# Kernel tuning notes

Hardware: AMD Instinct MI355X
Metric: run time of the kernel (lower is better)

The kernel has to match this reference:

```python
import jax, jax.numpy as jnp
import numpy as np

B, N, K, H = 4, 2048, 30, 8
NUM_HIDDEN, NUM_IN, NUM_LATENT = 512, 640, 128
D = NUM_HIDDEN // H


def setup_inputs() -> dict:
    key = jax.random.key(0)
    ks = jax.random.split(key, 10)
    s = 0.05
    return {
        "z": jax.random.normal(ks[0], (B, NUM_LATENT), jnp.float32),
        "h_V": jax.random.normal(ks[1], (B, N, NUM_HIDDEN), jnp.float32),
        "h_E": jax.random.normal(ks[2], (B, N, K, NUM_IN), jnp.float32),
        "mask_attend": jnp.ones((B, N, K), jnp.float32),
        # weights stored as (in, out); torch Linear computes x @ W.T
        "W_Q": jax.random.normal(ks[3], (NUM_HIDDEN, NUM_HIDDEN), jnp.float32) * s,
        "W_K": jax.random.normal(ks[4], (NUM_IN, NUM_HIDDEN), jnp.float32) * s,
        "W_V": jax.random.normal(ks[5], (NUM_IN, NUM_HIDDEN), jnp.float32) * s,
        "W_O": jax.random.normal(ks[6], (NUM_HIDDEN, NUM_HIDDEN), jnp.float32) * s,
        "W_z": jax.random.normal(ks[7], (NUM_LATENT, K * H), jnp.float32) * s,
        "W_b": jax.random.normal(ks[8], (NUM_IN - 33, H), jnp.float32) * s,
    }


def reference(z, h_V, h_E, mask_attend, W_Q, W_K, W_V, W_O, W_z, W_b):
    b, n, k, _ = h_E.shape
    # projections
    Q = (h_V @ W_Q).reshape(b, n, H, D)            # [B,N,H,D]
    Kp = (h_E @ W_K).reshape(b, n, k, H, D)        # [B,N,K,H,D]
    V = (h_E @ W_V).reshape(b, n, k, H, D)         # [B,N,K,H,D]
    # per-neighbor dot-product scores -> [B,N,H,K]
    logits = jnp.einsum("bnhd,bnkhd->bnhk", Q, Kp) / np.sqrt(D).astype(np.float32)
    # latent bias: W_z output reshaped as (K, H) then transposed -> [B,1,H,K]
    bias_latent = (z @ W_z).reshape(b, 1, k, H).transpose(0, 1, 3, 2)
    # edge bias from h_E features past index 33 -> [B,N,H,K]
    bias_edges = (h_E[..., 33:] @ W_b).reshape(b, n, k, H).transpose(0, 1, 3, 2)
    logits = logits + bias_latent + bias_edges
    # masked, numerically stable softmax over K neighbors
    mask = mask_attend[:, :, None, :]              # [B,N,1,K] broadcast over heads
    neg_inf = jnp.finfo(jnp.float32).min
    logits = jnp.where(mask > 0, logits, neg_inf)
    attend = jax.nn.softmax(logits, axis=-1) * mask  # [B,N,H,K]
    # weighted aggregation of V, merge heads, output projection
    h_upd = jnp.einsum("bnhk,bnkhd->bnhd", attend, V).reshape(b, n, NUM_HIDDEN)
    return h_upd @ W_O
```

## Files before the change

### kernel.cpp

```cpp
#include <hip/hip_runtime.h>

#define B_      4
#define N_      2048
#define KN      30
#define H_      8
#define D_      64
#define CH      512
#define CI      640
#define CL      128
#define BN_TOT  8192

typedef unsigned short u16;
typedef unsigned int   u32;

typedef __attribute__((ext_vector_type(8))) short bf16x8;
typedef __attribute__((ext_vector_type(4))) float f32x4;

__device__ __forceinline__ float bf2f(u16 u) {
    return __uint_as_float(((u32)u) << 16);
}
__device__ __forceinline__ u16 f2bf(float f) {
    u32 u = __float_as_uint(f);
    return (u16)((u + 0x7FFFu + ((u >> 16) & 1u)) >> 16);
}

#define NEG_INF (-3.4028234663852886e38f)

__device__ __forceinline__ void async16(const void* g, void* l) {
    __builtin_amdgcn_global_load_lds(
        (const __attribute__((address_space(1))) unsigned int*)g,
        (__attribute__((address_space(3))) unsigned int*)l, 16, 0, 0);
}

__global__ __launch_bounds__(256) void cvt_kernel(
    const float* __restrict__ in, u16* __restrict__ out, int n)
{
    int i4 = (blockIdx.x * 256 + threadIdx.x) * 4;
    if (i4 < n) {
        float4 v = *(const float4*)&in[i4];
        ushort4 s;
        s.x = f2bf(v.x); s.y = f2bf(v.y); s.z = f2bf(v.z); s.w = f2bf(v.w);
        *(ushort4*)&out[i4] = s;
    }
}

__global__ __launch_bounds__(256) void cvt_t_kernel(
    const float* __restrict__ in, u16* __restrict__ out, int R, int Cc)
{
    int o = blockIdx.x * 256 + threadIdx.x;
    if (o < R * Cc) {
        int j = o / R, i = o - j * R;
        out[o] = f2bf(in[(size_t)i * Cc + j]);
    }
}

template<int BN, bool BF16OUT, bool WBIAS>
__global__ __launch_bounds__(256) void mfma_gemm(
    const u16* __restrict__ A, const u16* __restrict__ Bt, void* __restrict__ Cp,
    int K, int lda, int ldb, int ldc,
    long aHead, long bHead, long cHead, float alpha,
    const float* __restrict__ wb)
{
    constexpr int WN = BN / 2;
    constexpr int NT = WN / 16;
    constexpr int BR = (BN * 4) / 256;

    __shared__ u16 lA[128 * 32];
    __shared__ u16 lB[BN * 32];

    const int t    = threadIdx.x;
    const int w    = t >> 6;
    const int lane = t & 63;
    const int fr   = lane & 15;
    const int fq   = lane >> 4;
    const int wm   = w >> 1, wn = w & 1;
    const int m0   = blockIdx.y * 128;
    const int n0   = blockIdx.x * BN;

    const u16* Ah = A  + (size_t)blockIdx.z * aHead;
    const u16* Bh = Bt + (size_t)blockIdx.z * bHead;

    f32x4 zero = {0.f, 0.f, 0.f, 0.f};
    f32x4 acc[4][NT];
#pragma unroll
    for (int i = 0; i < 4; i++)
#pragma unroll
        for (int j = 0; j < NT; j++) acc[i][j] = zero;

    for (int k0 = 0; k0 < K; k0 += 32) {
#pragma unroll
        for (int r = 0; r < 2; r++) {
            int chunk = r * 256 + t;
            async16(Ah + (size_t)(m0 + (chunk >> 2)) * lda + k0 + ((chunk & 3) << 3),
                    &lA[(r * 256 + w * 64) * 8]);
        }
#pragma unroll
        for (int r = 0; r < BR; r++) {
            int chunk = r * 256 + t;
            async16(Bh + (size_t)(n0 + (chunk >> 2)) * ldb + k0 + ((chunk & 3) << 3),
                    &lB[(r * 256 + w * 64) * 8]);
        }
        __syncthreads();

        bf16x8 af[4], bfr[NT];
#pragma unroll
        for (int i = 0; i < 4; i++)
            af[i] = *(const bf16x8*)&lA[(wm * 64 + i * 16 + fr) * 32 + fq * 8];
#pragma unroll
        for (int j = 0; j < NT; j++)
            bfr[j] = *(const bf16x8*)&lB[(wn * WN + j * 16 + fr) * 32 + fq * 8];
#pragma unroll
        for (int i = 0; i < 4; i++)
#pragma unroll
            for (int j = 0; j < NT; j++)
                acc[i][j] = __builtin_amdgcn_mfma_f32_16x16x32_bf16(
                    af[i], bfr[j], acc[i][j], 0, 0, 0);
        __syncthreads();
    }

    const size_t cbase = (size_t)blockIdx.z * cHead;
#pragma unroll
    for (int i = 0; i < 4; i++) {
        int row = m0 + wm * 64 + i * 16 + fq * 4;
#pragma unroll
        for (int j = 0; j < NT; j++) {
            int col = n0 + wn * WN + j * 16 + fr;
#pragma unroll
            for (int r = 0; r < 4; r++) {
                float v = acc[i][j][r] * alpha;
                if (WBIAS) {
                    if (col >= 33) v += wb[(size_t)(col - 33) * H_ + blockIdx.z];
                }
                if (BF16OUT)
                    ((u16*)Cp)[cbase + (size_t)(row + r) * ldc + col] = f2bf(v);
                else
                    ((float*)Cp)[cbase + (size_t)(row + r) * ldc + col] = v;
            }
        }
    }
}

__global__ __launch_bounds__(256) void biasl_kernel(
    const float* __restrict__ z, const float* __restrict__ Wz,
    float* __restrict__ biasL)
{
    const int t = threadIdx.x;
    if (t < KN * H_) {
        for (int b = 0; b < B_; b++) {
            float s = 0.f;
            for (int l = 0; l < CL; l++) s += z[b * CL + l] * Wz[l * (KN * H_) + t];
            biasL[b * (KN * H_) + t] = s;
        }
    }
}

__global__ __launch_bounds__(256) void attn_kernel(
    const float* __restrict__ hE, const float* __restrict__ mask,
    const u16* Qt, const float* __restrict__ biasL, u16* Eagg)
{
    __shared__ __align__(16) u16 ehs[KN * CI];
    __shared__ __align__(16) u16 lqt[H_ * CI];
    __shared__ float logit_s[H_ * 32];
    __shared__ float att_s[KN * H_];
    __shared__ float mask_s[KN];

    const int bn   = blockIdx.x;
    const int b    = bn >> 11;
    const int t    = threadIdx.x;
    const int w    = t >> 6;
    const int lane = t & 63;
    const int fr   = lane & 15;
    const int fq   = lane >> 4;
    char* ebase = (char*)ehs;
    char* qbase = (char*)lqt;

    const float* he = hE + (size_t)bn * KN * CI;
    {
        int idx = t;
#pragma unroll 6
        for (int it = 0; it < 18; ++it, idx += 256) {
            int k = idx / 160;
            int c = (idx - k * 160) << 2;
            float4 v = *(const float4*)&he[k * CI + c];
            ushort4 sv;
            sv.x = f2bf(v.x); sv.y = f2bf(v.y); sv.z = f2bf(v.z); sv.w = f2bf(v.w);
            *(ushort4*)(ebase + ((k * 1280 + (c << 1)) ^ ((k & 7) << 4))) = sv;
        }
        if (t < 192) {
            int idx2 = 4608 + t;
            int k = idx2 / 160;
            int c = (idx2 - k * 160) << 2;
            float4 v = *(const float4*)&he[k * CI + c];
            ushort4 sv;
            sv.x = f2bf(v.x); sv.y = f2bf(v.y); sv.z = f2bf(v.z); sv.w = f2bf(v.w);
            *(ushort4*)(ebase + ((k * 1280 + (c << 1)) ^ ((k & 7) << 4))) = sv;
        }
    }
    {
        const u16* qg = Qt + (size_t)bn * (H_ * CI);
        for (int idx = t; idx < 640; idx += 256) {
            int row = idx / 80;
            bf16x8 v = *(const bf16x8*)(qg + idx * 8);
            *(bf16x8*)(qbase + ((idx * 16) ^ ((row & 7) << 4))) = v;
        }
    }
    if (t < KN) mask_s[t] = mask[(size_t)bn * KN + t];
    __syncthreads();

    if (w < 2) {
        const int h8   = fr & 7;
        const int qswz = h8 << 4;
        int nr = w * 16 + fr;
        if (nr > KN - 1) nr = KN - 1;
        const char* erow = ebase + nr * 1280;
        const int swz = (nr & 7) << 4;
        f32x4 lacc = {0.f, 0.f, 0.f, 0.f};
#pragma unroll 4
        for (int kk = 0; kk < CI / 32; kk++) {
            bf16x8 a  = *(const bf16x8*)(qbase + ((h8 * 1280 + kk * 64 + fq * 16) ^ qswz));
            bf16x8 bf = *(const bf16x8*)(erow + ((kk * 64 + fq * 16) ^ swz));
            lacc = __builtin_amdgcn_mfma_f32_16x16x32_bf16(a, bf, lacc, 0, 0, 0);
        }
        int k = w * 16 + fr;
        if (fq < 2 && k < KN) {
            float mk = mask_s[k];
            const float* blp = &biasL[b * (KN * H_) + k * H_];
#pragma unroll
            for (int r = 0; r < 4; r++) {
                int h = fq * 4 + r;
                float lg = lacc[r] + blp[h];
                logit_s[h * 32 + k] = (mk > 0.f) ? lg : NEG_INF;
            }
        }
    }
    __syncthreads();

    if (t < 64) {
        const int h  = t >> 3;
        const int kg = t & 7;
        float lv[4];
#pragma unroll
        for (int i = 0; i < 4; i++) {
            int k = kg * 4 + i;
            float v = logit_s[h * 32 + k];
            lv[i] = (k < KN) ? v : NEG_INF;
        }
        float m = fmaxf(fmaxf(lv[0], lv[1]), fmaxf(lv[2], lv[3]));
        m = fmaxf(m, __shfl_xor(m, 1));
        m = fmaxf(m, __shfl_xor(m, 2));
        m = fmaxf(m, __shfl_xor(m, 4));
        float e[4], s = 0.f;
#pragma unroll
        for (int i = 0; i < 4; i++) { e[i] = __expf(lv[i] - m); s += e[i]; }
        s += __shfl_xor(s, 1);
        s += __shfl_xor(s, 2);
        s += __shfl_xor(s, 4);
        float inv = 1.f / s;
#pragma unroll
        for (int i = 0; i < 4; i++) {
            int k = kg * 4 + i;
            if (k < KN) att_s[k * H_ + h] = e[i] * inv * mask_s[k];
        }
    }
    __syncthreads();

    if (t < 160) {
        const int c0 = t << 2;
        float acc[8][4] = {};
        for (int k = 0; k < KN; k++) {
            ushort4 ev = *(const ushort4*)(ebase + ((k * 1280 + (c0 << 1)) ^ ((k & 7) << 4)));
            float f0 = bf2f(ev.x), f1 = bf2f(ev.y), f2 = bf2f(ev.z), f3 = bf2f(ev.w);
            float4 a0 = *(const float4*)&att_s[k * H_];
            float4 a1 = *(const float4*)&att_s[k * H_ + 4];
            float aw[8] = {a0.x, a0.y, a0.z, a0.w, a1.x, a1.y, a1.z, a1.w};
#pragma unroll
            for (int h = 0; h < 8; h++) {
                acc[h][0] += aw[h] * f0; acc[h][1] += aw[h] * f1;
                acc[h][2] += aw[h] * f2; acc[h][3] += aw[h] * f3;
            }
        }
#pragma unroll
        for (int h = 0; h < 8; h++) {
            ushort4 sv;
            sv.x = f2bf(acc[h][0]); sv.y = f2bf(acc[h][1]);
            sv.z = f2bf(acc[h][2]); sv.w = f2bf(acc[h][3]);
            *(ushort4*)&Eagg[((size_t)bn * H_ + h) * CI + c0] = sv;
        }
    }
}

extern "C" void kernel_launch(void* const* d_in, const int* in_sizes, int n_in,
                              void* d_out, int out_size, void* d_ws, size_t ws_size,
                              hipStream_t stream)
{
    const float* z    = (const float*)d_in[0];
    const float* hV   = (const float*)d_in[1];
    const float* hE   = (const float*)d_in[2];
    const float* mask = (const float*)d_in[3];
    const float* WQ   = (const float*)d_in[4];
    const float* WK   = (const float*)d_in[5];
    const float* WV   = (const float*)d_in[6];
    const float* WO   = (const float*)d_in[7];
    const float* Wz   = (const float*)d_in[8];
    const float* Wb   = (const float*)d_in[9];
    float* out = (float*)d_out;

    char* w = (char*)d_ws;
    u16*   hV_bf = (u16*)w;
    u16*   Q_bf  = (u16*)(w + 8388608);
    u16*   Qt    = (u16*)(w + 16777216);
    u16*   WQt   = (u16*)(w + 100663296);
    u16*   WK_bf = (u16*)(w + 101187584);
    u16*   WVt   = (u16*)(w + 101842944);
    u16*   WOt   = (u16*)(w + 102498304);
    float* biasL = (float*)(w + 103022592);
    u16*   Eagg  = Qt;
    u16*   Hupd  = hV_bf;

    cvt_kernel<<<4096, 256, 0, stream>>>(hV, hV_bf, BN_TOT * CH);
    cvt_kernel<<<320, 256, 0, stream>>>(WK, WK_bf, CI * CH);
    cvt_t_kernel<<<1024, 256, 0, stream>>>(WQ, WQt, CH, CH);
    cvt_t_kernel<<<1280, 256, 0, stream>>>(WV, WVt, CI, CH);
    cvt_t_kernel<<<1024, 256, 0, stream>>>(WO, WOt, CH, CH);
    biasl_kernel<<<1, 256, 0, stream>>>(z, Wz, biasL);

    mfma_gemm<128, true, false><<<dim3(4, 64, 1), 256, 0, stream>>>(
        hV_bf, WQt, Q_bf, CH, CH, CH, CH, 0, 0, 0, 1.0f, nullptr);
    mfma_gemm<128, true, true><<<dim3(5, 64, H_), 256, 0, stream>>>(
        Q_bf, WK_bf, Qt, 64, CH, CH, H_ * CI, 64, 64, CI, 0.125f, Wb);
    attn_kernel<<<dim3(BN_TOT), 256, 0, stream>>>(hE, mask, Qt, biasL, Eagg);
    mfma_gemm<64, true, false><<<dim3(1, 64, H_), 256, 0, stream>>>(
        Eagg, WVt, Hupd, CI, H_ * CI, CI, CH, CI, 64L * CI, 64, 1.0f, nullptr);
    mfma_gemm<128, false, false><<<dim3(4, 64, 1), 256, 0, stream>>>(
        Hupd, WOt, out, CH, CH, CH, CH, 0, 0, 0, 1.0f, nullptr);
}
```

Baseline: 1.061 ms.

## Use MFMA for attention-weighted edge aggregation and packed bf16 conversion in attn kernel

The per-node attention kernel now computes the weighted sum of edge features over 30 neighbours with bf16 MFMA (16x16x32) instead of scalar FP32 FMAs on 160 threads, storing attention weights as bf16 padded to 32 neighbours and 16 rows. Edge loading is reorganised so each thread handles a neighbour row, uses the packed v_cvt_pk_bf16_f32 conversion and a two-level XOR swizzle, and zero-fills padding rows. Q is read directly from global memory instead of being staged in LDS, which frees shared memory. Attention weights now pass through bf16, which loses some precision. The B operand is gathered with eight scalar 16-bit LDS reads per MFMA, and the output is written as scattered 16-bit stores.

```diff
diff --git a/kernel.cpp b/kernel.cpp
--- a/kernel.cpp
+++ b/kernel.cpp
@@ -23,6 +23,14 @@
     u32 u = __float_as_uint(f);
     return (u16)((u + 0x7FFFu + ((u >> 16) & 1u)) >> 16);
 }
+__device__ __forceinline__ u32 pk2bf(float lo, float hi) {
+    u32 r;
+    asm("v_cvt_pk_bf16_f32 %0, %1, %2" : "=v"(r) : "v"(lo), "v"(hi));
+    return r;
+}
+__device__ __forceinline__ u16 f2bf1(float f) {
+    return (u16)pk2bf(f, f);
+}
 
 #define NEG_INF (-3.4028234663852886e38f)
 
@@ -158,10 +166,9 @@
     const float* __restrict__ hE, const float* __restrict__ mask,
     const u16* Qt, const float* __restrict__ biasL, u16* Eagg)
 {
-    __shared__ __align__(16) u16 ehs[KN * CI];
-    __shared__ __align__(16) u16 lqt[H_ * CI];
+    __shared__ __align__(16) u16 ehs[32 * CI];
     __shared__ float logit_s[H_ * 32];
-    __shared__ float att_s[KN * H_];
+    __shared__ __align__(8) u16 att_b[16 * 32];
     __shared__ float mask_s[KN];
 
     const int bn   = blockIdx.x;
@@ -172,52 +179,44 @@
     const int fr   = lane & 15;
     const int fq   = lane >> 4;
     char* ebase = (char*)ehs;
-    char* qbase = (char*)lqt;
 
     const float* he = hE + (size_t)bn * KN * CI;
     {
-        int idx = t;
-#pragma unroll 6
-        for (int it = 0; it < 18; ++it, idx += 256) {
-            int k = idx / 160;
-            int c = (idx - k * 160) << 2;
-            float4 v = *(const float4*)&he[k * CI + c];
-            ushort4 sv;
-            sv.x = f2bf(v.x); sv.y = f2bf(v.y); sv.z = f2bf(v.z); sv.w = f2bf(v.w);
-            *(ushort4*)(ebase + ((k * 1280 + (c << 1)) ^ ((k & 7) << 4))) = sv;
-        }
-        if (t < 192) {
-            int idx2 = 4608 + t;
-            int k = idx2 / 160;
-            int c = (idx2 - k * 160) << 2;
-            float4 v = *(const float4*)&he[k * CI + c];
-            ushort4 sv;
-            sv.x = f2bf(v.x); sv.y = f2bf(v.y); sv.z = f2bf(v.z); sv.w = f2bf(v.w);
-            *(ushort4*)(ebase + ((k * 1280 + (c << 1)) ^ ((k & 7) << 4))) = sv;
-        }
-    }
-    {
-        const u16* qg = Qt + (size_t)bn * (H_ * CI);
-        for (int idx = t; idx < 640; idx += 256) {
-            int row = idx / 80;
-            bf16x8 v = *(const bf16x8*)(qg + idx * 8);
-            *(bf16x8*)(qbase + ((idx * 16) ^ ((row & 7) << 4))) = v;
+        const int kr = t >> 3;
+        const int c8 = t & 7;
+        char* wrow = ebase + kr * 1280;
+        const u32 swz = (u32)(((kr & 7) << 4) ^ ((kr & 24) << 2));
+        if (kr < KN) {
+            const float* hrow = he + kr * CI + c8 * 4;
+#pragma unroll 5
+            for (int i = 0; i < 20; i++) {
+                float4 v = *(const float4*)(hrow + i * 32);
+                uint2 p;
+                p.x = pk2bf(v.x, v.y);
+                p.y = pk2bf(v.z, v.w);
+                *(uint2*)(wrow + (((u32)((c8 + i * 8) * 8)) ^ swz)) = p;
+            }
+        } else {
+            uint2 zz; zz.x = 0u; zz.y = 0u;
+#pragma unroll 5
+            for (int i = 0; i < 20; i++)
+                *(uint2*)(wrow + (((u32)((c8 + i * 8) * 8)) ^ swz)) = zz;
         }
     }
     if (t < KN) mask_s[t] = mask[(size_t)bn * KN + t];
     __syncthreads();
 
     if (w < 2) {
-        const int h8   = fr & 7;
-        const int qswz = h8 << 4;
+        const int h8 = fr & 7;
+        const u16* qrow = Qt + (size_t)bn * (H_ * CI) + h8 * CI + fq * 8;
         int nr = w * 16 + fr;
         if (nr > KN - 1) nr = KN - 1;
         const char* erow = ebase + nr * 1280;
-        const int swz = (nr & 7) << 4;
+        const int swz = ((nr & 7) << 4) ^ ((nr & 24) << 2);
         f32x4 lacc = {0.f, 0.f, 0.f, 0.f};
 #pragma unroll 4
         for (int kk = 0; kk < CI / 32; kk++) {
-            bf16x8 a  = *(const bf16x8*)(qbase + ((h8 * 1280 + kk * 64 + fq * 16) ^ qswz));
+            bf16x8 a  = *(const bf16x8*)(qrow + kk * 32);
             bf16x8 bf = *(const bf16x8*)(erow + ((kk * 64 + fq * 16) ^ swz));
             lacc = __builtin_amdgcn_mfma_f32_16x16x32_bf16(a, bf, lacc, 0, 0, 0);
         }
@@ -256,35 +255,50 @@
         s += __shfl_xor(s, 2);
         s += __shfl_xor(s, 4);
         float inv = 1.f / s;
+        float av[4];
 #pragma unroll
         for (int i = 0; i < 4; i++) {
             int k = kg * 4 + i;
-            if (k < KN) att_s[k * H_ + h] = e[i] * inv * mask_s[k];
-        }
+            float mk = (k < KN) ? mask_s[k] : 0.f;
+            av[i] = e[i] * inv * mk;
+        }
+        uint2 p;
+        p.x = pk2bf(av[0], av[1]);
+        p.y = pk2bf(av[2], av[3]);
+        *(uint2*)&att_b[h * 32 + kg * 4] = p;
+    } else if (t < 128) {
+        const int u = t - 64;
+        uint2 zz; zz.x = 0u; zz.y = 0u;
+        *(uint2*)&att_b[(8 + (u >> 3)) * 32 + (u & 7) * 4] = zz;
     }
     __syncthreads();
 
-    if (t < 160) {
-        const int c0 = t << 2;
-        float acc[8][4] = {};
-        for (int k = 0; k < KN; k++) {
-            ushort4 ev = *(const ushort4*)(ebase + ((k * 1280 + (c0 << 1)) ^ ((k & 7) << 4)));
-            float f0 = bf2f(ev.x), f1 = bf2f(ev.y), f2 = bf2f(ev.z), f3 = bf2f(ev.w);
-            float4 a0 = *(const float4*)&att_s[k * H_];
-            float4 a1 = *(const float4*)&att_s[k * H_ + 4];
-            float aw[8] = {a0.x, a0.y, a0.z, a0.w, a1.x, a1.y, a1.z, a1.w};
-#pragma unroll
-            for (int h = 0; h < 8; h++) {
-                acc[h][0] += aw[h] * f0; acc[h][1] += aw[h] * f1;
-                acc[h][2] += aw[h] * f2; acc[h][3] += aw[h] * f3;
-            }
-        }
-#pragma unroll
-        for (int h = 0; h < 8; h++) {
-            ushort4 sv;
-            sv.x = f2bf(acc[h][0]); sv.y = f2bf(acc[h][1]);
-            sv.z = f2bf(acc[h][2]); sv.w = f2bf(acc[h][3]);
-            *(ushort4*)&Eagg[((size_t)bn * H_ + h) * CI + c0] = sv;
+    {
+        f32x4 zero4 = {0.f, 0.f, 0.f, 0.f};
+        bf16x8 afrag = *(const bf16x8*)&att_b[fr * 32 + fq * 8];
+        const u32 fqk  = (u32)(fq * 10240);
+        const u32 fqs  = (u32)(fq << 5);
+        const u32 colb = (u32)(w * 320 + fr * 2);
+        u16* outp = Eagg + (size_t)bn * (H_ * CI);
+#pragma unroll 2
+        for (int i = 0; i < 10; i++) {
+            const u32 cb = colb + (u32)(i * 32);
+            union { u16 u[8]; bf16x8 v; } bu;
+#pragma unroll
+            for (int j = 0; j < 8; j++) {
+                u32 a = ((fqk + (u32)(j * 1280) + cb) ^ ((u32)(j << 4))) ^ fqs;
+                bu.u[j] = *(const u16*)(ebase + a);
+            }
+            f32x4 d = __builtin_amdgcn_mfma_f32_16x16x32_bf16(
+                afrag, bu.v, zero4, 0, 0, 0);
+            if (fq < 2) {
+                int c = w * 160 + i * 16 + fr;
+#pragma unroll
+                for (int r = 0; r < 4; r++) {
+                    int h = fq * 4 + r;
+                    outp[h * CI + c] = f2bf1(d[r]);
+                }
+            }
         }
     }
 }
```

After: 1.052 ms. Within noise of the previous version (-0.9%).
